# Kernel optimization log

Hardware: AMD Instinct MI355X
Metric: run time of the kernel (lower is better)

## Reference

```python
import jax, jax.numpy as jnp
import numpy as np

B, T, C, H = 128, 512, 256, 64  # batch, seq (<= BLOCK_SIZE=512), EMBED_SIZE, HEAD_SIZE


def setup_inputs() -> dict:
    key = jax.random.key(0)
    k0, k1, k2, k3 = jax.random.split(key, 4)
    # nn.Linear(C, H, bias=False) applies x @ W.T with W:[H,C]; we store the
    # transposed weight [C,H] so the math x @ W is identical.
    scale = 1.0 / np.sqrt(C)  # rough Linear-init scale, values only matter for testing
    return {
        "input_embeddings": jax.random.normal(k0, (B, T, C), dtype=jnp.float32),
        "Wq": jax.random.normal(k1, (C, H), dtype=jnp.float32) * scale,
        "Wk": jax.random.normal(k2, (C, H), dtype=jnp.float32) * scale,
        "Wv": jax.random.normal(k3, (C, H), dtype=jnp.float32) * scale,
    }


def reference(input_embeddings, Wq, Wk, Wv):
    x = input_embeddings
    t = x.shape[1]
    h = Wq.shape[1]
    q = jnp.einsum("btc,ch->bth", x, Wq)
    k = jnp.einsum("btc,ch->bth", x, Wk)
    v = jnp.einsum("btc,ch->bth", x, Wv)
    # QK^T / sqrt(H), causal mask, softmax  (faithful to masked_fill(-inf))
    sim = jnp.einsum("bth,bsh->bts", q, k) / jnp.sqrt(jnp.asarray(h, x.dtype))
    causal = jnp.tril(jnp.ones((t, t), dtype=bool))
    sim = jnp.where(causal, sim, -jnp.inf)
    wei = jax.nn.softmax(sim, axis=-1)
    out = jnp.einsum("bts,bsh->bth", wei, v)
    return out
```

## Files before the change

### kernel.cpp

```cpp
#include <hip/hip_runtime.h>
#include <hip/hip_bf16.h>
#include <math.h>

#define Bn 128
#define Tn 512
#define Cn 256
#define Hn 64
#define HP2 72
#define SCL 0.18033688011112042f

typedef __attribute__((ext_vector_type(8))) short short8v;
typedef __attribute__((ext_vector_type(4))) float float4v;

__device__ __forceinline__ ushort f2bf(float f) {
    __hip_bfloat16 h = __float2bfloat16(f);
    return *reinterpret_cast<ushort*>(&h);
}

__global__ __launch_bounds__(256) void prep_w_kernel(
    const float* __restrict__ Wq, const float* __restrict__ Wk,
    const float* __restrict__ Wv, ushort* __restrict__ wcT3)
{
    const int row = blockIdx.x;
    const int c   = threadIdx.x;
    const int kc  = c >> 6;
    const int k2  = c & 63;
    const float* W = (row < 64) ? Wq : (row < 128) ? Wk : Wv;
    const int h = row & 63;
    wcT3[(kc * 192 + row) * 64 + (k2 ^ ((row & 7) << 3))] = f2bf(W[c * Hn + h]);
}

__global__ __launch_bounds__(256) void qkv_mfma_kernel(
    const float* __restrict__ x, const ushort* __restrict__ wcT3,
    ushort* __restrict__ q, ushort* __restrict__ k, ushort* __restrict__ vT)
{
    __shared__ char lds[81920];

    const int tid  = threadIdx.x;
    const int lane = tid & 63;
    const int wv   = tid >> 6;
    const int lr   = lane & 15;
    const int hi   = lane >> 4;
    const int wr   = wv >> 1;
    const int wc   = wv & 1;
    const long rows0 = (long)blockIdx.x * 128;

    {
        const char* gw = (const char*)wcT3;
        #pragma unroll
        for (int i = 0; i < 6; ++i) {
            int off = (wv * 6 + i) * 1024;
            __builtin_amdgcn_global_load_lds(
                (const __attribute__((address_space(1))) unsigned int*)(gw + off + (lane << 4)),
                (__attribute__((address_space(3))) unsigned int*)(lds + 32768 + off),
                16, 0, 0);
        }
    }
    {
        const float4* x4 = (const float4*)x;
        float4 xr[8];
        #pragma unroll
        for (int i = 0; i < 8; ++i) {
            int idx = tid + i * 256;
            int r   = idx >> 4;
            int f   = idx & 15;
            xr[i] = x4[(rows0 + r) * 64 + f];
        }
        #pragma unroll
        for (int i = 0; i < 8; ++i) {
            int idx = tid + i * 256;
            int r   = idx >> 4;
            int f   = idx & 15;
            union { ushort u[4]; uint2 p; } pk;
            pk.u[0] = f2bf(xr[i].x); pk.u[1] = f2bf(xr[i].y);
            pk.u[2] = f2bf(xr[i].z); pk.u[3] = f2bf(xr[i].w);
            *(uint2*)(lds + r * 128 + ((f * 8) ^ ((r & 7) << 4))) = pk.p;
        }
    }

    float4v acc[4][6];
    #pragma unroll
    for (int s = 0; s < 4; ++s)
        #pragma unroll
        for (int n = 0; n < 6; ++n) acc[s][n] = (float4v){0.f, 0.f, 0.f, 0.f};

    for (int c = 0; c < 4; ++c) {
        __syncthreads();

        const int par = c & 1;
        float4 xn[8];
        if (c < 3) {
            const char* gw = (const char*)wcT3 + (long)(c + 1) * 24576;
            #pragma unroll
            for (int i = 0; i < 6; ++i) {
                int off = (wv * 6 + i) * 1024;
                __builtin_amdgcn_global_load_lds(
                    (const __attribute__((address_space(1))) unsigned int*)(gw + off + (lane << 4)),
                    (__attribute__((address_space(3))) unsigned int*)(lds + 32768 + (1 - par) * 24576 + off),
                    16, 0, 0);
            }
            const float4* x4 = (const float4*)x;
            #pragma unroll
            for (int i = 0; i < 8; ++i) {
                int idx = tid + i * 256;
                int r   = idx >> 4;
                int f   = idx & 15;
                xn[i] = x4[(rows0 + r) * 64 + (c + 1) * 16 + f];
            }
        }

        const char* xb = lds + par * 16384;
        const char* wb = lds + 32768 + par * 24576;
        #pragma unroll
        for (int ks = 0; ks < 2; ++ks) {
            const int kb = ks * 64 + hi * 16;
            short8v a[4];
            #pragma unroll
            for (int s = 0; s < 4; ++s) {
                int r = wr * 64 + s * 16 + lr;
                a[s] = *(const short8v*)(xb + r * 128 + (kb ^ ((r & 7) << 4)));
            }
            #pragma unroll
            for (int n = 0; n < 6; ++n) {
                int wrow = wc * 96 + n * 16 + lr;
                short8v wf = *(const short8v*)(wb + wrow * 128 + (kb ^ ((wrow & 7) << 4)));
                #pragma unroll
                for (int s = 0; s < 4; ++s)
                    acc[s][n] = __builtin_amdgcn_mfma_f32_16x16x32_bf16(a[s], wf, acc[s][n], 0, 0, 0);
            }
        }

        if (c < 3) {
            char* xd = lds + (1 - par) * 16384;
            #pragma unroll
            for (int i = 0; i < 8; ++i) {
                int idx = tid + i * 256;
                int r   = idx >> 4;
                int f   = idx & 15;
                union { ushort u[4]; uint2 p; } pk;
                pk.u[0] = f2bf(xn[i].x); pk.u[1] = f2bf(xn[i].y);
                pk.u[2] = f2bf(xn[i].z); pk.u[3] = f2bf(xn[i].w);
                *(uint2*)(xd + r * 128 + ((f * 8) ^ ((r & 7) << 4))) = pk.p;
            }
        }
    }

    __syncthreads();

    #pragma unroll
    for (int s = 0; s < 4; ++s) {
        const int tb = wr * 64 + s * 16 + hi * 4;
        #pragma unroll
        for (int n = 0; n < 6; ++n) {
            const int col16 = wc * 96 + n * 16;
            if (col16 < 128) {
                char* qkb = lds + ((col16 < 64) ? 0 : 16384);
                int h = (col16 + lr) & 63;
                #pragma unroll
                for (int reg = 0; reg < 4; ++reg) {
                    int t = tb + reg;
                    *(ushort*)(qkb + t * 128 + ((h * 2) ^ ((t & 7) << 4))) =
                        f2bf(acc[s][n][reg]);
                }
            } else {
                int h = col16 - 128 + lr;
                ushort4 pk;
                pk.x = f2bf(acc[s][n][0]); pk.y = f2bf(acc[s][n][1]);
                pk.z = f2bf(acc[s][n][2]); pk.w = f2bf(acc[s][n][3]);
                *(ushort4*)(lds + 32768 + h * 256 + ((tb * 2) ^ ((h & 7) << 4))) = pk;
            }
        }
    }
    __syncthreads();

    {
        const int bb = (int)(rows0 >> 9);
        const int t0 = (int)(rows0 & 511);
        #pragma unroll
        for (int i = 0; i < 4; ++i) {
            int idx = tid + i * 256;
            int t   = idx >> 3;
            int f   = idx & 7;
            uint4 vq = *(const uint4*)(lds + t * 128 + ((f * 16) ^ ((t & 7) << 4)));
            *(uint4*)(q + (rows0 + t) * Hn + f * 8) = vq;
            uint4 vk = *(const uint4*)(lds + 16384 + t * 128 + ((f * 16) ^ ((t & 7) << 4)));
            *(uint4*)(k + (rows0 + t) * Hn + f * 8) = vk;
            int h  = idx >> 4;
            int fv = idx & 15;
            uint4 vv = *(const uint4*)(lds + 32768 + h * 256 + ((fv * 16) ^ ((h & 7) << 4)));
            *(uint4*)(vT + ((long)bb * Hn + h) * Tn + t0 + fv * 8) = vv;
        }
    }
}

__global__ __launch_bounds__(512) void attn_mfma_kernel(
    const ushort* __restrict__ q, const ushort* __restrict__ k,
    const ushort* __restrict__ vT, float* __restrict__ out)
{
    __shared__ ushort Ks[64 * HP2];
    __shared__ ushort Vt[64 * HP2];
    __shared__ ushort Pl[8][16 * HP2];

    const int tid = threadIdx.x;
    const int f   = blockIdx.x;
    const int c   = f & 255;
    const int b   = c >> 1;
    const int par = c & 1;
    const int qtp = (f < 256) ? par : (3 - par);
    const int ntiles = 2 * qtp + 2;

    const long base  = (long)b * Tn * Hn;
    const int lane = tid & 63;
    const int wv   = tid >> 6;
    const int lr   = lane & 15;
    const int hi   = lane >> 4;

    const int qrow_g = qtp * 128 + wv * 16;
    const int mrow0  = qrow_g + hi * 4;

    short8v qa[2];
    {
        const ushort* qp = q + base + (long)(qrow_g + lr) * Hn + hi * 8;
        qa[0] = *(const short8v*)(qp);
        qa[1] = *(const short8v*)(qp + 32);
    }

    const int sr  = tid >> 3;
    const int sc8 = tid & 7;
    uint4 kreg = *(const uint4*)(k + base + (long)sr * Hn + sc8 * 8);
    uint4 vreg = *(const uint4*)(vT + base + (long)sr * Tn + sc8 * 8);

    float4v o[4];
    #pragma unroll
    for (int n = 0; n < 4; ++n) o[n] = (float4v){0.f, 0.f, 0.f, 0.f};
    float m[4], l[4];
    #pragma unroll
    for (int reg = 0; reg < 4; ++reg) { m[reg] = -INFINITY; l[reg] = 0.f; }

    for (int kt = 0; kt < ntiles; ++kt) {
        __syncthreads();
        *(uint4*)&Ks[sr * HP2 + sc8 * 8] = kreg;
        *(uint4*)&Vt[sr * HP2 + sc8 * 8] = vreg;
        __syncthreads();
        if (kt + 1 < ntiles) {
            kreg = *(const uint4*)(k  + base + (long)((kt + 1) * 64 + sr) * Hn + sc8 * 8);
            vreg = *(const uint4*)(vT + base + (long)sr * Tn + (kt + 1) * 64 + sc8 * 8);
        }
        if (kt * 64 > qrow_g + 15) continue;

        float4v s4[4];
        #pragma unroll
        for (int n = 0; n < 4; ++n) s4[n] = (float4v){0.f, 0.f, 0.f, 0.f};
        #pragma unroll
        for (int ks = 0; ks < 2; ++ks) {
            short8v a = qa[ks];
            #pragma unroll
            for (int n = 0; n < 4; ++n) {
                short8v bb = *(const short8v*)&Ks[(n * 16 + lr) * HP2 + ks * 32 + hi * 8];
                s4[n] = __builtin_amdgcn_mfma_f32_16x16x32_bf16(a, bb, s4[n], 0, 0, 0);
            }
        }

        const bool partial = (kt * 64 + 63 > qrow_g);
        if (partial) {
            #pragma unroll
            for (int n = 0; n < 4; ++n) {
                int kcol = kt * 64 + n * 16 + lr;
                #pragma unroll
                for (int reg = 0; reg < 4; ++reg) {
                    float y = s4[n][reg] * SCL;
                    s4[n][reg] = (kcol <= mrow0 + reg) ? y : -INFINITY;
                }
            }
        } else {
            #pragma unroll
            for (int n = 0; n < 4; ++n)
                #pragma unroll
                for (int reg = 0; reg < 4; ++reg) s4[n][reg] *= SCL;
        }

        #pragma unroll
        for (int reg = 0; reg < 4; ++reg) {
            float mx = fmaxf(fmaxf(s4[0][reg], s4[1][reg]),
                             fmaxf(s4[2][reg], s4[3][reg]));
            mx = fmaxf(mx, __shfl_xor(mx, 1));
            mx = fmaxf(mx, __shfl_xor(mx, 2));
            mx = fmaxf(mx, __shfl_xor(mx, 4));
            mx = fmaxf(mx, __shfl_xor(mx, 8));
            float mN = fmaxf(m[reg], mx);
            float sc = exp2f(m[reg] - mN);
            float ps = 0.f;
            #pragma unroll
            for (int n = 0; n < 4; ++n) {
                float p = exp2f(s4[n][reg] - mN);
                s4[n][reg] = p;
                ps += p;
            }
            ps += __shfl_xor(ps, 1);
            ps += __shfl_xor(ps, 2);
            ps += __shfl_xor(ps, 4);
            ps += __shfl_xor(ps, 8);
            l[reg] = l[reg] * sc + ps;
            m[reg] = mN;
            #pragma unroll
            for (int n = 0; n < 4; ++n) o[n][reg] *= sc;
        }

        #pragma unroll
        for (int n = 0; n < 4; ++n)
            #pragma unroll
            for (int reg = 0; reg < 4; ++reg)
                Pl[wv][(hi * 4 + reg) * HP2 + n * 16 + lr] = f2bf(s4[n][reg]);

        #pragma unroll
        for (int ks = 0; ks < 2; ++ks) {
            short8v a = *(const short8v*)&Pl[wv][lr * HP2 + ks * 32 + hi * 8];
            #pragma unroll
            for (int n = 0; n < 4; ++n) {
                short8v bb = *(const short8v*)&Vt[(n * 16 + lr) * HP2 + ks * 32 + hi * 8];
                o[n] = __builtin_amdgcn_mfma_f32_16x16x32_bf16(a, bb, o[n], 0, 0, 0);
            }
        }
    }

    #pragma unroll
    for (int reg = 0; reg < 4; ++reg) {
        float inv = 1.0f / l[reg];
        float* orow = out + base + (long)(mrow0 + reg) * Hn;
        #pragma unroll
        for (int n = 0; n < 4; ++n)
            orow[n * 16 + lr] = o[n][reg] * inv;
    }
}

extern "C" void kernel_launch(void* const* d_in, const int* in_sizes, int n_in,
                              void* d_out, int out_size, void* d_ws, size_t ws_size,
                              hipStream_t stream) {
    const float* x  = (const float*)d_in[0];
    const float* Wq = (const float*)d_in[1];
    const float* Wk = (const float*)d_in[2];
    const float* Wv = (const float*)d_in[3];
    float* out = (float*)d_out;

    const size_t n = (size_t)Bn * Tn * Hn;
    ushort* qws  = (ushort*)d_ws;
    ushort* kws  = qws + n;
    ushort* vTs  = kws + n;
    ushort* wcT3 = vTs + n;

    prep_w_kernel<<<dim3(192), 256, 0, stream>>>(Wq, Wk, Wv, wcT3);
    qkv_mfma_kernel<<<dim3(512), 256, 0, stream>>>(x, wcT3, qws, kws, vTs);
    attn_mfma_kernel<<<dim3(512), 512, 0, stream>>>(qws, kws, vTs, out);
}
```

Baseline: 48.76 us.

## Split QKV projection across two blocks per row tile to raise occupancy

The QKV projection grid doubles from 512 to 1024 blocks. Each block now computes 96 output columns (Q plus half of V, or K plus the other half of V) instead of 192, and the weight prep kernel is rewritten to lay out weights in matching halves. LDS use drops from 80KB to 40KB and the accumulator count halves, which should allow more resident blocks per CU and better latency hiding. In exchange, each x tile is read and converted to bf16 twice, the x staging loses its double buffering and gains an extra barrier per k-chunk, and paired blocks are interleaved so both read the same x tile close together in time.

```diff
diff --git a/kernel.cpp b/kernel.cpp
--- a/kernel.cpp
+++ b/kernel.cpp
@@ -19,22 +19,28 @@
 
 __global__ __launch_bounds__(256) void prep_w_kernel(
     const float* __restrict__ Wq, const float* __restrict__ Wk,
-    const float* __restrict__ Wv, ushort* __restrict__ wcT3)
+    const float* __restrict__ Wv, ushort* __restrict__ wcT4)
 {
-    const int row = blockIdx.x;
+    const int g   = blockIdx.x;
+    const int nh  = g / 96;
+    const int row = g % 96;
     const int c   = threadIdx.x;
     const int kc  = c >> 6;
     const int k2  = c & 63;
-    const float* W = (row < 64) ? Wq : (row < 128) ? Wk : Wv;
-    const int h = row & 63;
-    wcT3[(kc * 192 + row) * 64 + (k2 ^ ((row & 7) << 3))] = f2bf(W[c * Hn + h]);
+    const float* W;
+    int h;
+    if (row < 64) { W = nh ? Wk : Wq; h = row; }
+    else          { W = Wv; h = nh * 32 + (row - 64); }
+    wcT4[(((nh * 4 + kc) * 96) + row) * 64 + (k2 ^ ((row & 7) << 3))] =
+        f2bf(W[c * Hn + h]);
 }
 
 __global__ __launch_bounds__(256) void qkv_mfma_kernel(
-    const float* __restrict__ x, const ushort* __restrict__ wcT3,
+    const float* __restrict__ x, const ushort* __restrict__ wcT4,
     ushort* __restrict__ q, ushort* __restrict__ k, ushort* __restrict__ vT)
 {
-    __shared__ char lds[81920];
+    __shared__ char lds[40960];
+    const int WOFF = 16384;
 
     const int tid  = threadIdx.x;
     const int lane = tid & 63;
@@ -43,74 +49,71 @@
     const int hi   = lane >> 4;
     const int wr   = wv >> 1;
     const int wc   = wv & 1;
-    const long rows0 = (long)blockIdx.x * 128;
-
-    {
-        const char* gw = (const char*)wcT3;
-        #pragma unroll
-        for (int i = 0; i < 6; ++i) {
-            int off = (wv * 6 + i) * 1024;
-            __builtin_amdgcn_global_load_lds(
-                (const __attribute__((address_space(1))) unsigned int*)(gw + off + (lane << 4)),
-                (__attribute__((address_space(3))) unsigned int*)(lds + 32768 + off),
-                16, 0, 0);
-        }
-    }
-    {
-        const float4* x4 = (const float4*)x;
-        float4 xr[8];
+
+    const int bid     = blockIdx.x;
+    const int nh      = (bid >> 3) & 1;
+    const int rowtile = (bid & 7) | ((bid >> 4) << 3);
+    const long rows0  = (long)rowtile * 128;
+
+    const char* gw = (const char*)wcT4 + (long)nh * 4 * 12288;
+    const float4* x4 = (const float4*)x;
+
+    #pragma unroll
+    for (int i = 0; i < 3; ++i) {
+        int off = (wv * 3 + i) * 1024;
+        __builtin_amdgcn_global_load_lds(
+            (const __attribute__((address_space(1))) unsigned int*)(gw + off + (lane << 4)),
+            (__attribute__((address_space(3))) unsigned int*)(lds + WOFF + off),
+            16, 0, 0);
+    }
+    float4 xr[8];
+    #pragma unroll
+    for (int i = 0; i < 8; ++i) {
+        int idx = tid + i * 256;
+        int r = idx >> 4, f = idx & 15;
+        xr[i] = x4[(rows0 + r) * 64 + f];
+    }
+
+    float4v acc[4][3];
+    #pragma unroll
+    for (int s = 0; s < 4; ++s)
+        #pragma unroll
+        for (int n = 0; n < 3; ++n) acc[s][n] = (float4v){0.f, 0.f, 0.f, 0.f};
+
+    for (int kc = 0; kc < 4; ++kc) {
+        const int par = kc & 1;
+        __syncthreads();
+
         #pragma unroll
         for (int i = 0; i < 8; ++i) {
             int idx = tid + i * 256;
-            int r   = idx >> 4;
-            int f   = idx & 15;
-            xr[i] = x4[(rows0 + r) * 64 + f];
-        }
-        #pragma unroll
-        for (int i = 0; i < 8; ++i) {
-            int idx = tid + i * 256;
-            int r   = idx >> 4;
-            int f   = idx & 15;
+            int r = idx >> 4, f = idx & 15;
             union { ushort u[4]; uint2 p; } pk;
             pk.u[0] = f2bf(xr[i].x); pk.u[1] = f2bf(xr[i].y);
             pk.u[2] = f2bf(xr[i].z); pk.u[3] = f2bf(xr[i].w);
             *(uint2*)(lds + r * 128 + ((f * 8) ^ ((r & 7) << 4))) = pk.p;
         }
-    }
-
-    float4v acc[4][6];
-    #pragma unroll
-    for (int s = 0; s < 4; ++s)
-        #pragma unroll
-        for (int n = 0; n < 6; ++n) acc[s][n] = (float4v){0.f, 0.f, 0.f, 0.f};
-
-    for (int c = 0; c < 4; ++c) {
         __syncthreads();
 
-        const int par = c & 1;
-        float4 xn[8];
-        if (c < 3) {
-            const char* gw = (const char*)wcT3 + (long)(c + 1) * 24576;
-            #pragma unroll
-            for (int i = 0; i < 6; ++i) {
-                int off = (wv * 6 + i) * 1024;
+        if (kc < 3) {
+            const char* gw2 = gw + (kc + 1) * 12288;
+            #pragma unroll
+            for (int i = 0; i < 3; ++i) {
+                int off = (wv * 3 + i) * 1024;
                 __builtin_amdgcn_global_load_lds(
-                    (const __attribute__((address_space(1))) unsigned int*)(gw + off + (lane << 4)),
-                    (__attribute__((address_space(3))) unsigned int*)(lds + 32768 + (1 - par) * 24576 + off),
+                    (const __attribute__((address_space(1))) unsigned int*)(gw2 + off + (lane << 4)),
+                    (__attribute__((address_space(3))) unsigned int*)(lds + WOFF + (1 - par) * 12288 + off),
                     16, 0, 0);
             }
-            const float4* x4 = (const float4*)x;
             #pragma unroll
             for (int i = 0; i < 8; ++i) {
                 int idx = tid + i * 256;
-                int r   = idx >> 4;
-                int f   = idx & 15;
-                xn[i] = x4[(rows0 + r) * 64 + (c + 1) * 16 + f];
-            }
-        }
-
-        const char* xb = lds + par * 16384;
-        const char* wb = lds + 32768 + par * 24576;
+                int r = idx >> 4, f = idx & 15;
+                xr[i] = x4[(rows0 + r) * 64 + (kc + 1) * 16 + f];
+            }
+        }
+
+        const char* wb = lds + WOFF + par * 12288;
         #pragma unroll
         for (int ks = 0; ks < 2; ++ks) {
             const int kb = ks * 64 + hi * 16;
@@ -118,31 +121,17 @@
             #pragma unroll
             for (int s = 0; s < 4; ++s) {
                 int r = wr * 64 + s * 16 + lr;
-                a[s] = *(const short8v*)(xb + r * 128 + (kb ^ ((r & 7) << 4)));
-            }
-            #pragma unroll
-            for (int n = 0; n < 6; ++n) {
-                int wrow = wc * 96 + n * 16 + lr;
+                a[s] = *(const short8v*)(lds + r * 128 + (kb ^ ((r & 7) << 4)));
+            }
+            #pragma unroll
+            for (int n = 0; n < 3; ++n) {
+                int wrow = wc * 48 + n * 16 + lr;
                 short8v wf = *(const short8v*)(wb + wrow * 128 + (kb ^ ((wrow & 7) << 4)));
                 #pragma unroll
                 for (int s = 0; s < 4; ++s)
                     acc[s][n] = __builtin_amdgcn_mfma_f32_16x16x32_bf16(a[s], wf, acc[s][n], 0, 0, 0);
             }
         }
-
-        if (c < 3) {
-            char* xd = lds + (1 - par) * 16384;
-            #pragma unroll
-            for (int i = 0; i < 8; ++i) {
-                int idx = tid + i * 256;
-                int r   = idx >> 4;
-                int f   = idx & 15;
-                union { ushort u[4]; uint2 p; } pk;
-                pk.u[0] = f2bf(xn[i].x); pk.u[1] = f2bf(xn[i].y);
-                pk.u[2] = f2bf(xn[i].z); pk.u[3] = f2bf(xn[i].w);
-                *(uint2*)(xd + r * 128 + ((f * 8) ^ ((r & 7) << 4))) = pk.p;
-            }
-        }
     }
 
     __syncthreads();
@@ -151,23 +140,22 @@
     for (int s = 0; s < 4; ++s) {
         const int tb = wr * 64 + s * 16 + hi * 4;
         #pragma unroll
-        for (int n = 0; n < 6; ++n) {
-            const int col16 = wc * 96 + n * 16;
-            if (col16 < 128) {
-                char* qkb = lds + ((col16 < 64) ? 0 : 16384);
-                int h = (col16 + lr) & 63;
+        for (int n = 0; n < 3; ++n) {
+            const int col16 = wc * 48 + n * 16;
+            if (col16 < 64) {
+                int h = col16 + lr;
                 #pragma unroll
                 for (int reg = 0; reg < 4; ++reg) {
                     int t = tb + reg;
-                    *(ushort*)(qkb + t * 128 + ((h * 2) ^ ((t & 7) << 4))) =
+                    *(ushort*)(lds + t * 128 + ((h * 2) ^ ((t & 7) << 4))) =
                         f2bf(acc[s][n][reg]);
                 }
             } else {
-                int h = col16 - 128 + lr;
+                int hl = col16 - 64 + lr;
                 ushort4 pk;
                 pk.x = f2bf(acc[s][n][0]); pk.y = f2bf(acc[s][n][1]);
                 pk.z = f2bf(acc[s][n][2]); pk.w = f2bf(acc[s][n][3]);
-                *(ushort4*)(lds + 32768 + h * 256 + ((tb * 2) ^ ((h & 7) << 4))) = pk;
+                *(ushort4*)(lds + WOFF + hl * 256 + ((tb * 2) ^ ((hl & 7) << 4))) = pk;
             }
         }
     }
@@ -176,19 +164,20 @@
     {
         const int bb = (int)(rows0 >> 9);
         const int t0 = (int)(rows0 & 511);
+        ushort* qk = nh ? k : q;
         #pragma unroll
         for (int i = 0; i < 4; ++i) {
             int idx = tid + i * 256;
-            int t   = idx >> 3;
-            int f   = idx & 7;
-            uint4 vq = *(const uint4*)(lds + t * 128 + ((f * 16) ^ ((t & 7) << 4)));
-            *(uint4*)(q + (rows0 + t) * Hn + f * 8) = vq;
-            uint4 vk = *(const uint4*)(lds + 16384 + t * 128 + ((f * 16) ^ ((t & 7) << 4)));
-            *(uint4*)(k + (rows0 + t) * Hn + f * 8) = vk;
-            int h  = idx >> 4;
-            int fv = idx & 15;
-            uint4 vv = *(const uint4*)(lds + 32768 + h * 256 + ((fv * 16) ^ ((h & 7) << 4)));
-            *(uint4*)(vT + ((long)bb * Hn + h) * Tn + t0 + fv * 8) = vv;
+            int t = idx >> 3, f = idx & 7;
+            uint4 w = *(const uint4*)(lds + t * 128 + ((f * 16) ^ ((t & 7) << 4)));
+            *(uint4*)(qk + (rows0 + t) * Hn + f * 8) = w;
+        }
+        #pragma unroll
+        for (int i = 0; i < 2; ++i) {
+            int idx = tid + i * 256;
+            int hl = idx >> 4, fv = idx & 15;
+            uint4 w = *(const uint4*)(lds + WOFF + hl * 256 + ((fv * 16) ^ ((hl & 7) << 4)));
+            *(uint4*)(vT + ((long)bb * Hn + nh * 32 + hl) * Tn + t0 + fv * 8) = w;
         }
     }
 }
@@ -346,9 +335,9 @@
     ushort* qws  = (ushort*)d_ws;
     ushort* kws  = qws + n;
     ushort* vTs  = kws + n;
-    ushort* wcT3 = vTs + n;
-
-    prep_w_kernel<<<dim3(192), 256, 0, stream>>>(Wq, Wk, Wv, wcT3);
-    qkv_mfma_kernel<<<dim3(512), 256, 0, stream>>>(x, wcT3, qws, kws, vTs);
+    ushort* wcT4 = vTs + n;
+
+    prep_w_kernel<<<dim3(192), 256, 0, stream>>>(Wq, Wk, Wv, wcT4);
+    qkv_mfma_kernel<<<dim3(1024), 256, 0, stream>>>(x, wcT4, qws, kws, vTs);
     attn_mfma_kernel<<<dim3(512), 512, 0, stream>>>(qws, kws, vTs, out);
 }
```

New measurement: 49.41 us. About the same (+1.3%).
